# Optimization experiments

Hardware: AMD Instinct MI355X
Metric: run time of the kernel (lower is better)

The kernel has to match this reference:

```python
import jax, jax.numpy as jnp
import numpy as np

LOG2 = float(np.log(2.0))


def setup_inputs() -> dict:
    key = jax.random.key(0)
    ks = jax.random.split(key, 10)
    V, G, F, T = 262144, 4096, 256, 2
    node_feats = jax.random.normal(ks[0], (V, F), dtype=jnp.float32)
    segment_ids = jnp.sort(jax.random.randint(ks[1], (V,), 0, G))
    s = 0.05
    return {
        "node_feats": node_feats,
        "segment_ids": segment_ids,
        "num_graphs": G,
        "logit_w": jax.random.normal(ks[2], (T, 2 * F, 1), dtype=jnp.float32) * s,
        "logit_b": jnp.zeros((T, 1), dtype=jnp.float32),
        "proj_w": jax.random.normal(ks[3], (T, F, F), dtype=jnp.float32) * s,
        "proj_b": jnp.zeros((T, F), dtype=jnp.float32),
        "gru_w_ih": jax.random.normal(ks[4], (T, 3 * F, F), dtype=jnp.float32) * s,
        "gru_w_hh": jax.random.normal(ks[5], (T, 3 * F, F), dtype=jnp.float32) * s,
        "gru_b_ih": jnp.zeros((T, 3 * F), dtype=jnp.float32),
        "gru_b_hh": jnp.zeros((T, 3 * F), dtype=jnp.float32),
    }


def _gru_cell(x, h, w_ih, w_hh, b_ih, b_hh):
    # torch.nn.GRUCell math
    gi = x @ w_ih.T + b_ih  # [G, 3F]
    gh = h @ w_hh.T + b_hh
    i_r, i_z, i_n = jnp.split(gi, 3, axis=-1)
    h_r, h_z, h_n = jnp.split(gh, 3, axis=-1)
    r = jax.nn.sigmoid(i_r + h_r)
    z = jax.nn.sigmoid(i_z + h_z)
    n = jnp.tanh(i_n + r * h_n)
    return (1.0 - z) * n + z * h


def reference(node_feats, segment_ids, num_graphs, logit_w, logit_b,
              proj_w, proj_b, gru_w_ih, gru_w_hh, gru_b_ih, gru_b_hh):
    G = int(num_graphs)
    # initial graph feats: sum of node feats per graph
    g_feats = jax.ops.segment_sum(node_feats, segment_ids, num_segments=G)
    T = logit_w.shape[0]
    for t in range(T):
        # broadcast relu(g_feats) to nodes, concat with node feats, compute logits
        ctx_nodes = jax.nn.relu(g_feats)[segment_ids]              # [V, F]
        z = jnp.concatenate([ctx_nodes, node_feats], axis=-1) @ logit_w[t] + logit_b[t]  # [V,1]
        z = jnp.logaddexp(z, 0.0) - LOG2                           # SoftPlus2
        # segment softmax over nodes within each graph
        zmax = jax.ops.segment_max(z, segment_ids, num_segments=G)
        e = jnp.exp(z - zmax[segment_ids])
        denom = jax.ops.segment_sum(e, segment_ids, num_segments=G)
        a = e / denom[segment_ids]                                 # [V,1]
        # project nodes (dropout=0) and attention-weighted sum per graph
        hv = node_feats @ proj_w[t] + proj_b[t]                    # [V, F]
        g_repr = jax.ops.segment_sum(a * hv, segment_ids, num_segments=G)
        context = jax.nn.elu(g_repr)
        g_feats = _gru_cell(context, g_feats, gru_w_ih[t], gru_w_hh[t], gru_b_ih[t], gru_b_hh[t])
    return g_feats
```

## Files before the change

kernel.cpp:

```cpp
#include <hip/hip_runtime.h>
#include <hip/hip_bf16.h>
#include <math.h>

#define V_NODES 262144
#define NGRAPH  4096
#define FD      256
#define TSTEPS  2

typedef unsigned short u16;
typedef __attribute__((ext_vector_type(8))) short short8;
typedef __attribute__((ext_vector_type(4))) float f32x4;

__device__ __forceinline__ float bf2f(u16 u) {
  union { unsigned int i; float f; } x; x.i = ((unsigned int)u) << 16; return x.f;
}
__device__ __forceinline__ u16 f2bf(float f) {
  union { unsigned int i; float f; } x; x.f = f;
  unsigned int r = x.i + 0x7FFFu + ((x.i >> 16) & 1u);
  return (u16)(r >> 16);
}
__device__ __forceinline__ float softplus2(float x) {
  return fmaxf(x, 0.0f) + log1pf(__expf(-fabsf(x))) - 0.69314718056f;
}

__global__ void k_bounds(const int* __restrict__ seg, int* __restrict__ start) {
  int v = blockIdx.x * blockDim.x + threadIdx.x;
  if (v >= V_NODES) return;
  int s = seg[v];
  if (v == 0) {
    for (int g = 0; g <= s; ++g) start[g] = 0;
  } else {
    int p = seg[v - 1];
    for (int g = p + 1; g <= s; ++g) start[g] = v;
  }
  if (v == V_NODES - 1) {
    for (int g = s + 1; g <= NGRAPH; ++g) start[g] = V_NODES;
  }
}

__global__ __launch_bounds__(256) void k_pass1(
    const float* __restrict__ nf, const int* __restrict__ start,
    const float* __restrict__ logit_w,
    float* __restrict__ gf, u16* __restrict__ nbf,
    u16* __restrict__ hhi, u16* __restrict__ hlo,
    float* __restrict__ d0, float* __restrict__ d1) {
  __shared__ float red[4][FD];
  const int g = blockIdx.x, tid = threadIdx.x;
  const int wv = tid >> 6, l = tid & 63;
  const int s = start[g], e = start[g + 1];
  const float4 wA = ((const float4*)(logit_w + FD))[l];
  const float4 wB = ((const float4*)(logit_w + 512 + FD))[l];
  float a0 = 0.f, a1 = 0.f, a2 = 0.f, a3 = 0.f;
  const float4* nfv = (const float4*)nf;
  ushort4* nbv = (ushort4*)nbf;
  for (int v = s + wv; v < e; v += 4) {
    const float4 x = nfv[(size_t)v * 64 + l];
    a0 += x.x; a1 += x.y; a2 += x.z; a3 += x.w;
    ushort4 ub;
    ub.x = f2bf(x.x); ub.y = f2bf(x.y); ub.z = f2bf(x.z); ub.w = f2bf(x.w);
    nbv[(size_t)v * 64 + l] = ub;
    float dA = fmaf(x.x, wA.x, fmaf(x.y, wA.y, fmaf(x.z, wA.z, x.w * wA.w)));
    float dB = fmaf(x.x, wB.x, fmaf(x.y, wB.y, fmaf(x.z, wB.z, x.w * wB.w)));
#pragma unroll
    for (int off = 1; off < 64; off <<= 1) {
      dA += __shfl_xor(dA, off, 64);
      dB += __shfl_xor(dB, off, 64);
    }
    if (l == 0) { d0[v] = dA; d1[v] = dB; }
  }
  red[wv][l * 4 + 0] = a0; red[wv][l * 4 + 1] = a1;
  red[wv][l * 4 + 2] = a2; red[wv][l * 4 + 3] = a3;
  __syncthreads();
  const float sum = red[0][tid] + red[1][tid] + red[2][tid] + red[3][tid];
  const size_t idx = (size_t)g * FD + tid;
  gf[idx] = sum;
  const u16 hi = f2bf(sum);
  hhi[idx] = hi;
  hlo[idx] = f2bf(sum - bf2f(hi));
}

__global__ __launch_bounds__(256) void k_attnw(
    const int* __restrict__ start, const float* __restrict__ gf,
    const float* __restrict__ lwA, const float* __restrict__ lbp,
    const float* __restrict__ dt, float* __restrict__ abuf,
    float* __restrict__ den) {
  const int tid = threadIdx.x, lane = tid & 63, wv = tid >> 6;
  const int g = blockIdx.x * 4 + wv;
  const int s = start[g], e = start[g + 1];
  const float lb = lbp[0];
  const float4 hv = ((const float4*)(gf + (size_t)g * FD))[lane];
  const float4 wa = ((const float4*)lwA)[lane];
  float c = fmaf(fmaxf(hv.x, 0.f), wa.x, fmaf(fmaxf(hv.y, 0.f), wa.y,
            fmaf(fmaxf(hv.z, 0.f), wa.z, fmaxf(hv.w, 0.f) * wa.w)));
#pragma unroll
  for (int off = 1; off < 64; off <<= 1) c += __shfl_xor(c, off, 64);
  float m = -1e30f;
  for (int v = s + lane; v < e; v += 64) {
    const float z = softplus2(c + dt[v] + lb);
    abuf[v] = z;
    m = fmaxf(m, z);
  }
#pragma unroll
  for (int off = 1; off < 64; off <<= 1) m = fmaxf(m, __shfl_xor(m, off, 64));
  float lsum = 0.f;
  for (int v = s + lane; v < e; v += 64) {
    const float ez = __expf(abuf[v] - m);
    abuf[v] = ez;
    lsum += ez;
  }
#pragma unroll
  for (int off = 1; off < 64; off <<= 1) lsum += __shfl_xor(lsum, off, 64);
  if (lane == 0) den[g] = lsum;
}

__global__ __launch_bounds__(256) void k_wsum(
    const u16* __restrict__ nbf, const int* __restrict__ start,
    const float* __restrict__ abuf, const float* __restrict__ den,
    u16* __restrict__ wnsbf) {
  __shared__ float red[4][FD];
  const int g = blockIdx.x, tid = threadIdx.x;
  const int wv = tid >> 6, lane = tid & 63;
  const int half = lane >> 5, fl = lane & 31;
  const int s = start[g], e = start[g + 1];
  float acc[8];
#pragma unroll
  for (int j = 0; j < 8; ++j) acc[j] = 0.f;
  for (int v0 = s + 2 * wv + half; v0 < e; v0 += 8) {
    const uint4 u = ((const uint4*)(nbf + (size_t)v0 * FD))[fl];
    const float ev = abuf[v0];
    acc[0] = fmaf(ev, bf2f((u16)(u.x & 0xffff)), acc[0]);
    acc[1] = fmaf(ev, bf2f((u16)(u.x >> 16)),    acc[1]);
    acc[2] = fmaf(ev, bf2f((u16)(u.y & 0xffff)), acc[2]);
    acc[3] = fmaf(ev, bf2f((u16)(u.y >> 16)),    acc[3]);
    acc[4] = fmaf(ev, bf2f((u16)(u.z & 0xffff)), acc[4]);
    acc[5] = fmaf(ev, bf2f((u16)(u.z >> 16)),    acc[5]);
    acc[6] = fmaf(ev, bf2f((u16)(u.w & 0xffff)), acc[6]);
    acc[7] = fmaf(ev, bf2f((u16)(u.w >> 16)),    acc[7]);
  }
#pragma unroll
  for (int j = 0; j < 8; ++j) acc[j] += __shfl_xor(acc[j], 32, 64);
  if (half == 0) {
#pragma unroll
    for (int j = 0; j < 8; ++j) red[wv][fl * 8 + j] = acc[j];
  }
  __syncthreads();
  const float num = red[0][tid] + red[1][tid] + red[2][tid] + red[3][tid];
  const float dv = den[g];
  wnsbf[(size_t)g * FD + tid] = f2bf((e > s) ? (num / dv) : 0.0f);
}

__global__ void k_cvt(const float* __restrict__ src, u16* __restrict__ dst, int n4) {
  const int i = blockIdx.x * 256 + threadIdx.x;
  if (i >= n4) return;
  const float4 x = ((const float4*)src)[i];
  ushort4 u;
  u.x = f2bf(x.x); u.y = f2bf(x.y); u.z = f2bf(x.z); u.w = f2bf(x.w);
  ((ushort4*)dst)[i] = u;
}

__global__ void k_cvt_split(const float* __restrict__ src, u16* __restrict__ hi,
                            u16* __restrict__ lo, int n) {
  const int i = blockIdx.x * 256 + threadIdx.x;
  if (i >= n) return;
  const float x = src[i];
  const u16 h = f2bf(x);
  hi[i] = h;
  lo[i] = f2bf(x - bf2f(h));
}

__global__ void k_cvt_t(const float* __restrict__ src, u16* __restrict__ dst) {
  __shared__ float tile[32][33];
  const int t = blockIdx.z;
  const float* S = src + (size_t)t * FD * FD;
  u16* D = dst + (size_t)t * FD * FD;
  const int bx = blockIdx.x, by = blockIdx.y;
  const int tx = threadIdx.x, ty = threadIdx.y;
#pragma unroll
  for (int i = 0; i < 32; i += 8)
    tile[ty + i][tx] = S[(size_t)(by * 32 + ty + i) * FD + bx * 32 + tx];
  __syncthreads();
#pragma unroll
  for (int i = 0; i < 32; i += 8)
    D[(size_t)(bx * 32 + ty + i) * FD + by * 32 + tx] = f2bf(tile[tx][ty + i]);
}

template <int ACT, int OUTBF, int SPLIT>
__global__ __launch_bounds__(256) void k_wgemm(
    const u16* __restrict__ Xhi, const u16* __restrict__ Xlo,
    const u16* __restrict__ Whi, const u16* __restrict__ Wlo,
    const float* __restrict__ bias, float* __restrict__ Yf,
    u16* __restrict__ Ybf, int N) {
  const int tid = threadIdx.x, lane = tid & 63, wave = tid >> 6;
  const int mt = blockIdx.y * 4 + wave;
  const int nt = blockIdx.x;
  const int r = lane & 15, q = lane >> 4;
  const u16* xp = Xhi + (size_t)(mt * 16 + r) * FD + q * 8;
  const u16* wp = Whi + (size_t)(nt * 16 + r) * FD + q * 8;
  f32x4 acc = {0.f, 0.f, 0.f, 0.f};
#pragma unroll
  for (int kt = 0; kt < 8; ++kt) {
    const short8 a = *(const short8*)(xp + kt * 32);
    const short8 b = *(const short8*)(wp + kt * 32);
    acc = __builtin_amdgcn_mfma_f32_16x16x32_bf16(a, b, acc, 0, 0, 0);
  }
  if (SPLIT >= 1) {
    const u16* xp2 = Xlo + (size_t)(mt * 16 + r) * FD + q * 8;
#pragma unroll
    for (int kt = 0; kt < 8; ++kt) {
      const short8 a = *(const short8*)(xp2 + kt * 32);
      const short8 b = *(const short8*)(wp + kt * 32);
      acc = __builtin_amdgcn_mfma_f32_16x16x32_bf16(a, b, acc, 0, 0, 0);
    }
  }
  if (SPLIT >= 2) {
    const u16* wp2 = Wlo + (size_t)(nt * 16 + r) * FD + q * 8;
#pragma unroll
    for (int kt = 0; kt < 8; ++kt) {
      const short8 a = *(const short8*)(xp + kt * 32);
      const short8 b = *(const short8*)(wp2 + kt * 32);
      acc = __builtin_amdgcn_mfma_f32_16x16x32_bf16(a, b, acc, 0, 0, 0);
    }
  }
  const int gcol = nt * 16 + r;
  const float bs = bias[gcol];
  const int row0 = mt * 16 + q * 4;
#pragma unroll
  for (int i = 0; i < 4; ++i) {
    float v = acc[i] + bs;
    if (ACT == 1) v = (v > 0.0f) ? v : expm1f(v);
    if (OUTBF) Ybf[(size_t)(row0 + i) * N + gcol] = f2bf(v);
    else       Yf[(size_t)(row0 + i) * N + gcol] = v;
  }
}

__global__ __launch_bounds__(256) void k_gru(
    const float* __restrict__ gi, const float* __restrict__ gh,
    float* __restrict__ h, u16* __restrict__ hhi, u16* __restrict__ hlo) {
  const int g = blockIdx.x, f = threadIdx.x;
  const float* gir = gi + (size_t)g * 768;
  const float* ghr = gh + (size_t)g * 768;
  const float ir = gir[f], iz = gir[256 + f], in_ = gir[512 + f];
  const float hr = ghr[f], hz = ghr[256 + f], hn = ghr[512 + f];
  const float r = 1.0f / (1.0f + __expf(-(ir + hr)));
  const float z = 1.0f / (1.0f + __expf(-(iz + hz)));
  const float n = tanhf(in_ + r * hn);
  const size_t idx = (size_t)g * FD + f;
  const float hv = h[idx];
  const float hnew = (1.0f - z) * n + z * hv;
  h[idx] = hnew;
  const u16 hb = f2bf(hnew);
  hhi[idx] = hb;
  hlo[idx] = f2bf(hnew - bf2f(hb));
}

extern "C" void kernel_launch(void* const* d_in, const int* in_sizes, int n_in,
                              void* d_out, int out_size, void* d_ws, size_t ws_size,
                              hipStream_t stream) {
  const float* node    = (const float*)d_in[0];
  const int*   seg     = (const int*)d_in[1];
  const float* logit_w = (const float*)d_in[3];
  const float* logit_b = (const float*)d_in[4];
  const float* proj_w  = (const float*)d_in[5];
  const float* proj_b  = (const float*)d_in[6];
  const float* w_ih    = (const float*)d_in[7];
  const float* w_hh    = (const float*)d_in[8];
  const float* b_ih    = (const float*)d_in[9];
  const float* b_hh    = (const float*)d_in[10];
  float* gfeats = (float*)d_out;

  char* p = (char*)d_ws;
  int* start   = (int*)p;  p += (((NGRAPH + 1) * sizeof(int)) + 255) & ~(size_t)255;
  u16* nbf     = (u16*)p;  p += (size_t)V_NODES * FD * 2;
  float* d0    = (float*)p; p += (size_t)V_NODES * 4;
  float* d1    = (float*)p; p += (size_t)V_NODES * 4;
  float* abuf  = (float*)p; p += (size_t)V_NODES * 4;
  float* den   = (float*)p; p += (size_t)NGRAPH * 4;
  u16* hhi     = (u16*)p;  p += (size_t)NGRAPH * FD * 2;
  u16* hlo     = (u16*)p;  p += (size_t)NGRAPH * FD * 2;
  u16* wnsbf   = (u16*)p;  p += (size_t)NGRAPH * FD * 2;
  u16* ctxbf   = (u16*)p;  p += (size_t)NGRAPH * FD * 2;
  float* gi    = (float*)p; p += (size_t)NGRAPH * 768 * 4;
  float* gh    = (float*)p; p += (size_t)NGRAPH * 768 * 4;
  u16* wihbf   = (u16*)p;  p += (size_t)TSTEPS * 768 * FD * 2;
  u16* whhbf   = (u16*)p;  p += (size_t)TSTEPS * 768 * FD * 2;
  u16* whhlo   = (u16*)p;  p += (size_t)TSTEPS * 768 * FD * 2;
  u16* pwtbf   = (u16*)p;  p += (size_t)TSTEPS * FD * FD * 2;
  (void)ws_size; (void)in_sizes; (void)n_in; (void)out_size;

  k_bounds<<<dim3(V_NODES / 256), dim3(256), 0, stream>>>(seg, start);
  k_pass1<<<dim3(NGRAPH), dim3(256), 0, stream>>>(node, start, logit_w,
                                                  gfeats, nbf, hhi, hlo, d0, d1);

  const int nw = TSTEPS * 768 * FD;
  k_cvt<<<dim3(nw / 4 / 256), dim3(256), 0, stream>>>(w_ih, wihbf, nw / 4);
  k_cvt_split<<<dim3(nw / 256), dim3(256), 0, stream>>>(w_hh, whhbf, whhlo, nw);
  k_cvt_t<<<dim3(8, 8, TSTEPS), dim3(32, 8), 0, stream>>>(proj_w, pwtbf);

  for (int t = 0; t < TSTEPS; ++t) {
    k_attnw<<<dim3(NGRAPH / 4), dim3(256), 0, stream>>>(
        start, gfeats, logit_w + (size_t)t * 512, logit_b + t,
        (t == 0) ? d0 : d1, abuf, den);
    k_wsum<<<dim3(NGRAPH), dim3(256), 0, stream>>>(nbf, start, abuf, den, wnsbf);
    k_wgemm<1, 1, 0><<<dim3(FD / 16, NGRAPH / 64), dim3(256), 0, stream>>>(
        wnsbf, nullptr, pwtbf + (size_t)t * FD * FD, nullptr,
        proj_b + (size_t)t * FD, nullptr, ctxbf, FD);
    k_wgemm<0, 0, 0><<<dim3(768 / 16, NGRAPH / 64), dim3(256), 0, stream>>>(
        ctxbf, nullptr, wihbf + (size_t)t * 768 * FD, nullptr,
        b_ih + (size_t)t * 768, gi, nullptr, 768);
    k_wgemm<0, 0, 2><<<dim3(768 / 16, NGRAPH / 64), dim3(256), 0, stream>>>(
        hhi, hlo, whhbf + (size_t)t * 768 * FD, whhlo + (size_t)t * 768 * FD,
        b_hh + (size_t)t * 768, gh, nullptr, 768);
    k_gru<<<dim3(NGRAPH), dim3(256), 0, stream>>>(gi, gh, gfeats, hhi, hlo);
  }
}
```

Before: 643.5 us.

## Fuse all stages into one persistent megakernel with grid-wide barriers

```diff
diff --git a/kernel.cpp b/kernel.cpp
--- a/kernel.cpp
+++ b/kernel.cpp
@@ -6,6 +6,7 @@
 #define NGRAPH  4096
 #define FD      256
 #define TSTEPS  2
+#define NBLK    1024
 
 typedef unsigned short u16;
 typedef __attribute__((ext_vector_type(8))) short short8;
@@ -19,238 +20,288 @@
   unsigned int r = x.i + 0x7FFFu + ((x.i >> 16) & 1u);
   return (u16)(r >> 16);
 }
+__device__ __forceinline__ unsigned int pkbf(float a, float b) {
+  return (unsigned int)f2bf(a) | ((unsigned int)f2bf(b) << 16);
+}
 __device__ __forceinline__ float softplus2(float x) {
   return fmaxf(x, 0.0f) + log1pf(__expf(-fabsf(x))) - 0.69314718056f;
 }
 
-__global__ void k_bounds(const int* __restrict__ seg, int* __restrict__ start) {
-  int v = blockIdx.x * blockDim.x + threadIdx.x;
-  if (v >= V_NODES) return;
-  int s = seg[v];
-  if (v == 0) {
-    for (int g = 0; g <= s; ++g) start[g] = 0;
-  } else {
-    int p = seg[v - 1];
-    for (int g = p + 1; g <= s; ++g) start[g] = v;
-  }
-  if (v == V_NODES - 1) {
-    for (int g = s + 1; g <= NGRAPH; ++g) start[g] = V_NODES;
-  }
-}
-
-__global__ __launch_bounds__(256) void k_pass1(
-    const float* __restrict__ nf, const int* __restrict__ start,
-    const float* __restrict__ logit_w,
-    float* __restrict__ gf, u16* __restrict__ nbf,
-    u16* __restrict__ hhi, u16* __restrict__ hlo,
-    float* __restrict__ d0, float* __restrict__ d1) {
-  __shared__ float red[4][FD];
-  const int g = blockIdx.x, tid = threadIdx.x;
-  const int wv = tid >> 6, l = tid & 63;
-  const int s = start[g], e = start[g + 1];
-  const float4 wA = ((const float4*)(logit_w + FD))[l];
-  const float4 wB = ((const float4*)(logit_w + 512 + FD))[l];
-  float a0 = 0.f, a1 = 0.f, a2 = 0.f, a3 = 0.f;
-  const float4* nfv = (const float4*)nf;
-  ushort4* nbv = (ushort4*)nbf;
-  for (int v = s + wv; v < e; v += 4) {
-    const float4 x = nfv[(size_t)v * 64 + l];
-    a0 += x.x; a1 += x.y; a2 += x.z; a3 += x.w;
-    ushort4 ub;
-    ub.x = f2bf(x.x); ub.y = f2bf(x.y); ub.z = f2bf(x.z); ub.w = f2bf(x.w);
-    nbv[(size_t)v * 64 + l] = ub;
-    float dA = fmaf(x.x, wA.x, fmaf(x.y, wA.y, fmaf(x.z, wA.z, x.w * wA.w)));
-    float dB = fmaf(x.x, wB.x, fmaf(x.y, wB.y, fmaf(x.z, wB.z, x.w * wB.w)));
-#pragma unroll
-    for (int off = 1; off < 64; off <<= 1) {
-      dA += __shfl_xor(dA, off, 64);
-      dB += __shfl_xor(dB, off, 64);
-    }
-    if (l == 0) { d0[v] = dA; d1[v] = dB; }
-  }
-  red[wv][l * 4 + 0] = a0; red[wv][l * 4 + 1] = a1;
-  red[wv][l * 4 + 2] = a2; red[wv][l * 4 + 3] = a3;
+__device__ __forceinline__ void gsync(int* bar, int id) {
   __syncthreads();
-  const float sum = red[0][tid] + red[1][tid] + red[2][tid] + red[3][tid];
-  const size_t idx = (size_t)g * FD + tid;
-  gf[idx] = sum;
-  const u16 hi = f2bf(sum);
-  hhi[idx] = hi;
-  hlo[idx] = f2bf(sum - bf2f(hi));
-}
-
-__global__ __launch_bounds__(256) void k_attnw(
-    const int* __restrict__ start, const float* __restrict__ gf,
-    const float* __restrict__ lwA, const float* __restrict__ lbp,
-    const float* __restrict__ dt, float* __restrict__ abuf,
-    float* __restrict__ den) {
-  const int tid = threadIdx.x, lane = tid & 63, wv = tid >> 6;
-  const int g = blockIdx.x * 4 + wv;
-  const int s = start[g], e = start[g + 1];
-  const float lb = lbp[0];
-  const float4 hv = ((const float4*)(gf + (size_t)g * FD))[lane];
-  const float4 wa = ((const float4*)lwA)[lane];
-  float c = fmaf(fmaxf(hv.x, 0.f), wa.x, fmaf(fmaxf(hv.y, 0.f), wa.y,
-            fmaf(fmaxf(hv.z, 0.f), wa.z, fmaxf(hv.w, 0.f) * wa.w)));
-#pragma unroll
-  for (int off = 1; off < 64; off <<= 1) c += __shfl_xor(c, off, 64);
-  float m = -1e30f;
-  for (int v = s + lane; v < e; v += 64) {
-    const float z = softplus2(c + dt[v] + lb);
-    abuf[v] = z;
-    m = fmaxf(m, z);
-  }
-#pragma unroll
-  for (int off = 1; off < 64; off <<= 1) m = fmaxf(m, __shfl_xor(m, off, 64));
-  float lsum = 0.f;
-  for (int v = s + lane; v < e; v += 64) {
-    const float ez = __expf(abuf[v] - m);
-    abuf[v] = ez;
-    lsum += ez;
-  }
-#pragma unroll
-  for (int off = 1; off < 64; off <<= 1) lsum += __shfl_xor(lsum, off, 64);
-  if (lane == 0) den[g] = lsum;
-}
-
-__global__ __launch_bounds__(256) void k_wsum(
-    const u16* __restrict__ nbf, const int* __restrict__ start,
-    const float* __restrict__ abuf, const float* __restrict__ den,
-    u16* __restrict__ wnsbf) {
-  __shared__ float red[4][FD];
-  const int g = blockIdx.x, tid = threadIdx.x;
-  const int wv = tid >> 6, lane = tid & 63;
-  const int half = lane >> 5, fl = lane & 31;
-  const int s = start[g], e = start[g + 1];
-  float acc[8];
-#pragma unroll
-  for (int j = 0; j < 8; ++j) acc[j] = 0.f;
-  for (int v0 = s + 2 * wv + half; v0 < e; v0 += 8) {
-    const uint4 u = ((const uint4*)(nbf + (size_t)v0 * FD))[fl];
-    const float ev = abuf[v0];
-    acc[0] = fmaf(ev, bf2f((u16)(u.x & 0xffff)), acc[0]);
-    acc[1] = fmaf(ev, bf2f((u16)(u.x >> 16)),    acc[1]);
-    acc[2] = fmaf(ev, bf2f((u16)(u.y & 0xffff)), acc[2]);
-    acc[3] = fmaf(ev, bf2f((u16)(u.y >> 16)),    acc[3]);
-    acc[4] = fmaf(ev, bf2f((u16)(u.z & 0xffff)), acc[4]);
-    acc[5] = fmaf(ev, bf2f((u16)(u.z >> 16)),    acc[5]);
-    acc[6] = fmaf(ev, bf2f((u16)(u.w & 0xffff)), acc[6]);
-    acc[7] = fmaf(ev, bf2f((u16)(u.w >> 16)),    acc[7]);
-  }
-#pragma unroll
-  for (int j = 0; j < 8; ++j) acc[j] += __shfl_xor(acc[j], 32, 64);
-  if (half == 0) {
-#pragma unroll
-    for (int j = 0; j < 8; ++j) red[wv][fl * 8 + j] = acc[j];
+  if (threadIdx.x == 0) {
+    __threadfence();
+    __hip_atomic_fetch_add(&bar[id], 1, __ATOMIC_ACQ_REL, __HIP_MEMORY_SCOPE_AGENT);
+    while (__hip_atomic_load(&bar[id], __ATOMIC_ACQUIRE, __HIP_MEMORY_SCOPE_AGENT) < NBLK)
+      __builtin_amdgcn_s_sleep(2);
+    __threadfence();
   }
   __syncthreads();
-  const float num = red[0][tid] + red[1][tid] + red[2][tid] + red[3][tid];
-  const float dv = den[g];
-  wnsbf[(size_t)g * FD + tid] = f2bf((e > s) ? (num / dv) : 0.0f);
-}
-
-__global__ void k_cvt(const float* __restrict__ src, u16* __restrict__ dst, int n4) {
-  const int i = blockIdx.x * 256 + threadIdx.x;
-  if (i >= n4) return;
-  const float4 x = ((const float4*)src)[i];
-  ushort4 u;
-  u.x = f2bf(x.x); u.y = f2bf(x.y); u.z = f2bf(x.z); u.w = f2bf(x.w);
-  ((ushort4*)dst)[i] = u;
-}
-
-__global__ void k_cvt_split(const float* __restrict__ src, u16* __restrict__ hi,
-                            u16* __restrict__ lo, int n) {
-  const int i = blockIdx.x * 256 + threadIdx.x;
-  if (i >= n) return;
-  const float x = src[i];
-  const u16 h = f2bf(x);
-  hi[i] = h;
-  lo[i] = f2bf(x - bf2f(h));
-}
-
-__global__ void k_cvt_t(const float* __restrict__ src, u16* __restrict__ dst) {
-  __shared__ float tile[32][33];
-  const int t = blockIdx.z;
-  const float* S = src + (size_t)t * FD * FD;
-  u16* D = dst + (size_t)t * FD * FD;
-  const int bx = blockIdx.x, by = blockIdx.y;
-  const int tx = threadIdx.x, ty = threadIdx.y;
-#pragma unroll
-  for (int i = 0; i < 32; i += 8)
-    tile[ty + i][tx] = S[(size_t)(by * 32 + ty + i) * FD + bx * 32 + tx];
-  __syncthreads();
-#pragma unroll
-  for (int i = 0; i < 32; i += 8)
-    D[(size_t)(bx * 32 + ty + i) * FD + by * 32 + tx] = f2bf(tile[tx][ty + i]);
-}
-
-template <int ACT, int OUTBF, int SPLIT>
-__global__ __launch_bounds__(256) void k_wgemm(
-    const u16* __restrict__ Xhi, const u16* __restrict__ Xlo,
-    const u16* __restrict__ Whi, const u16* __restrict__ Wlo,
-    const float* __restrict__ bias, float* __restrict__ Yf,
-    u16* __restrict__ Ybf, int N) {
-  const int tid = threadIdx.x, lane = tid & 63, wave = tid >> 6;
-  const int mt = blockIdx.y * 4 + wave;
-  const int nt = blockIdx.x;
-  const int r = lane & 15, q = lane >> 4;
-  const u16* xp = Xhi + (size_t)(mt * 16 + r) * FD + q * 8;
-  const u16* wp = Whi + (size_t)(nt * 16 + r) * FD + q * 8;
-  f32x4 acc = {0.f, 0.f, 0.f, 0.f};
+}
+
+__device__ __forceinline__ f32x4 mm256(const u16* __restrict__ X,
+                                       const u16* __restrict__ W, f32x4 acc) {
 #pragma unroll
   for (int kt = 0; kt < 8; ++kt) {
-    const short8 a = *(const short8*)(xp + kt * 32);
-    const short8 b = *(const short8*)(wp + kt * 32);
+    const short8 a = *(const short8*)(X + kt * 32);
+    const short8 b = *(const short8*)(W + kt * 32);
     acc = __builtin_amdgcn_mfma_f32_16x16x32_bf16(a, b, acc, 0, 0, 0);
   }
-  if (SPLIT >= 1) {
-    const u16* xp2 = Xlo + (size_t)(mt * 16 + r) * FD + q * 8;
-#pragma unroll
-    for (int kt = 0; kt < 8; ++kt) {
-      const short8 a = *(const short8*)(xp2 + kt * 32);
-      const short8 b = *(const short8*)(wp + kt * 32);
-      acc = __builtin_amdgcn_mfma_f32_16x16x32_bf16(a, b, acc, 0, 0, 0);
-    }
-  }
-  if (SPLIT >= 2) {
-    const u16* wp2 = Wlo + (size_t)(nt * 16 + r) * FD + q * 8;
-#pragma unroll
-    for (int kt = 0; kt < 8; ++kt) {
-      const short8 a = *(const short8*)(xp + kt * 32);
-      const short8 b = *(const short8*)(wp2 + kt * 32);
-      acc = __builtin_amdgcn_mfma_f32_16x16x32_bf16(a, b, acc, 0, 0, 0);
-    }
-  }
-  const int gcol = nt * 16 + r;
-  const float bs = bias[gcol];
-  const int row0 = mt * 16 + q * 4;
-#pragma unroll
-  for (int i = 0; i < 4; ++i) {
-    float v = acc[i] + bs;
-    if (ACT == 1) v = (v > 0.0f) ? v : expm1f(v);
-    if (OUTBF) Ybf[(size_t)(row0 + i) * N + gcol] = f2bf(v);
-    else       Yf[(size_t)(row0 + i) * N + gcol] = v;
-  }
-}
-
-__global__ __launch_bounds__(256) void k_gru(
-    const float* __restrict__ gi, const float* __restrict__ gh,
-    float* __restrict__ h, u16* __restrict__ hhi, u16* __restrict__ hlo) {
-  const int g = blockIdx.x, f = threadIdx.x;
-  const float* gir = gi + (size_t)g * 768;
-  const float* ghr = gh + (size_t)g * 768;
-  const float ir = gir[f], iz = gir[256 + f], in_ = gir[512 + f];
-  const float hr = ghr[f], hz = ghr[256 + f], hn = ghr[512 + f];
-  const float r = 1.0f / (1.0f + __expf(-(ir + hr)));
-  const float z = 1.0f / (1.0f + __expf(-(iz + hz)));
-  const float n = tanhf(in_ + r * hn);
-  const size_t idx = (size_t)g * FD + f;
-  const float hv = h[idx];
-  const float hnew = (1.0f - z) * n + z * hv;
-  h[idx] = hnew;
-  const u16 hb = f2bf(hnew);
-  hhi[idx] = hb;
-  hlo[idx] = f2bf(hnew - bf2f(hb));
+  return acc;
+}
+
+__global__ __launch_bounds__(256, 4) void k_mega(
+    const float* __restrict__ nf, const int* __restrict__ seg,
+    const float* __restrict__ logit_w, const float* __restrict__ logit_b,
+    const float* __restrict__ proj_w, const float* __restrict__ proj_b,
+    const float* __restrict__ w_ih, const float* __restrict__ w_hh,
+    const float* __restrict__ b_ih, const float* __restrict__ b_hh,
+    float* __restrict__ gf, int* __restrict__ bar, int* __restrict__ start,
+    u16* __restrict__ nbf, float* __restrict__ d0, float* __restrict__ d1,
+    float* __restrict__ abuf, u16* __restrict__ hhi, u16* __restrict__ hlo,
+    u16* __restrict__ wnsbf, u16* __restrict__ ctxbf,
+    float* __restrict__ gibuf, float* __restrict__ ghbuf,
+    u16* __restrict__ wihbf, u16* __restrict__ whhbf, u16* __restrict__ whhlo,
+    u16* __restrict__ pwtbf) {
+  __shared__ char smem[8 * FD * 4];
+  __shared__ float sden[4];
+  float* redf = (float*)smem;
+  const int b = blockIdx.x, tid = threadIdx.x;
+  const int gtid = b * 256 + tid;
+  const int lane = tid & 63, wv = tid >> 6;
+
+  {
+    const int v = gtid;
+    const int s = seg[v];
+    if (v == 0) {
+      for (int g = 0; g <= s; ++g) start[g] = 0;
+    } else {
+      const int p = seg[v - 1];
+      for (int g = p + 1; g <= s; ++g) start[g] = v;
+    }
+    if (v == V_NODES - 1)
+      for (int g = s + 1; g <= NGRAPH; ++g) start[g] = V_NODES;
+  }
+  {
+    const int nchunk = TSTEPS * 768 * FD / 4;
+    if (gtid < nchunk) {
+      const float4 x = ((const float4*)w_ih)[gtid];
+      uint2 u; u.x = pkbf(x.x, x.y); u.y = pkbf(x.z, x.w);
+      ((uint2*)wihbf)[gtid] = u;
+      const float4 y = ((const float4*)w_hh)[gtid];
+      uint2 hi_, lo_;
+      const u16 h0 = f2bf(y.x), h1 = f2bf(y.y), h2 = f2bf(y.z), h3 = f2bf(y.w);
+      hi_.x = (unsigned)h0 | ((unsigned)h1 << 16);
+      hi_.y = (unsigned)h2 | ((unsigned)h3 << 16);
+      lo_.x = pkbf(y.x - bf2f(h0), y.y - bf2f(h1));
+      lo_.y = pkbf(y.z - bf2f(h2), y.w - bf2f(h3));
+      ((uint2*)whhbf)[gtid] = hi_;
+      ((uint2*)whhlo)[gtid] = lo_;
+    }
+  }
+  if (b < 2 * 64) {
+    float (*tl)[33] = (float(*)[33])smem;
+    const int t = b >> 6, tile = b & 63, bx = tile & 7, by = tile >> 3;
+    const int tx = tid & 31, ty = tid >> 5;
+    const float* S = proj_w + (size_t)t * FD * FD;
+    u16* D = pwtbf + (size_t)t * FD * FD;
+#pragma unroll
+    for (int i = 0; i < 32; i += 8)
+      tl[ty + i][tx] = S[(size_t)(by * 32 + ty + i) * FD + bx * 32 + tx];
+    __syncthreads();
+#pragma unroll
+    for (int i = 0; i < 32; i += 8)
+      D[(size_t)(bx * 32 + ty + i) * FD + by * 32 + tx] = f2bf(tl[tx][ty + i]);
+  }
+  gsync(bar, 0);
+
+  {
+    const int h = tid >> 5, sl = tid & 31;
+    float wA[8], wB[8];
+    {
+      const float4 a0 = ((const float4*)(logit_w + FD))[2 * sl];
+      const float4 a1 = ((const float4*)(logit_w + FD))[2 * sl + 1];
+      const float4 b0 = ((const float4*)(logit_w + 512 + FD))[2 * sl];
+      const float4 b1 = ((const float4*)(logit_w + 512 + FD))[2 * sl + 1];
+      wA[0]=a0.x; wA[1]=a0.y; wA[2]=a0.z; wA[3]=a0.w;
+      wA[4]=a1.x; wA[5]=a1.y; wA[6]=a1.z; wA[7]=a1.w;
+      wB[0]=b0.x; wB[1]=b0.y; wB[2]=b0.z; wB[3]=b0.w;
+      wB[4]=b1.x; wB[5]=b1.y; wB[6]=b1.z; wB[7]=b1.w;
+    }
+    for (int gl = 0; gl < 4; ++gl) {
+      const int g = b * 4 + gl;
+      const int s = start[g], e = start[g + 1];
+      float ac[8];
+#pragma unroll
+      for (int j = 0; j < 8; ++j) ac[j] = 0.f;
+      const float4* nfv = (const float4*)nf;
+      for (int v = s + h; v < e; v += 8) {
+        const float4 x0 = nfv[(size_t)v * 64 + 2 * sl];
+        const float4 x1 = nfv[(size_t)v * 64 + 2 * sl + 1];
+        ac[0]+=x0.x; ac[1]+=x0.y; ac[2]+=x0.z; ac[3]+=x0.w;
+        ac[4]+=x1.x; ac[5]+=x1.y; ac[6]+=x1.z; ac[7]+=x1.w;
+        uint4 u;
+        u.x = pkbf(x0.x, x0.y); u.y = pkbf(x0.z, x0.w);
+        u.z = pkbf(x1.x, x1.y); u.w = pkbf(x1.z, x1.w);
+        ((uint4*)(nbf + (size_t)v * FD))[sl] = u;
+        float dA = fmaf(x0.x, wA[0], fmaf(x0.y, wA[1], fmaf(x0.z, wA[2], x0.w * wA[3])));
+        dA = fmaf(x1.x, wA[4], fmaf(x1.y, wA[5], fmaf(x1.z, wA[6], fmaf(x1.w, wA[7], dA))));
+        float dB = fmaf(x0.x, wB[0], fmaf(x0.y, wB[1], fmaf(x0.z, wB[2], x0.w * wB[3])));
+        dB = fmaf(x1.x, wB[4], fmaf(x1.y, wB[5], fmaf(x1.z, wB[6], fmaf(x1.w, wB[7], dB))));
+#pragma unroll
+        for (int off = 1; off < 32; off <<= 1) {
+          dA += __shfl_xor(dA, off, 64);
+          dB += __shfl_xor(dB, off, 64);
+        }
+        if (sl == 0) { d0[v] = dA; d1[v] = dB; }
+      }
+      ((float4*)&redf[h * FD + sl * 8])[0] = make_float4(ac[0], ac[1], ac[2], ac[3]);
+      ((float4*)&redf[h * FD + sl * 8])[1] = make_float4(ac[4], ac[5], ac[6], ac[7]);
+      __syncthreads();
+      float sum = 0.f;
+#pragma unroll
+      for (int j = 0; j < 8; ++j) sum += redf[j * FD + tid];
+      const size_t idx = (size_t)g * FD + tid;
+      gf[idx] = sum;
+      const u16 hb = f2bf(sum);
+      hhi[idx] = hb;
+      hlo[idx] = f2bf(sum - bf2f(hb));
+      __syncthreads();
+    }
+  }
+
+  for (int t = 0; t < TSTEPS; ++t) {
+    __syncthreads();
+    {
+      const int g = b * 4 + wv;
+      const int s = start[g], e = start[g + 1];
+      const float lb = logit_b[t];
+      const float* dt = t ? d1 : d0;
+      const float4 hv = ((const float4*)gf)[(size_t)g * 64 + lane];
+      const float4 wa = ((const float4*)(logit_w + (size_t)t * 512))[lane];
+      float c = fmaf(fmaxf(hv.x, 0.f), wa.x, fmaf(fmaxf(hv.y, 0.f), wa.y,
+                fmaf(fmaxf(hv.z, 0.f), wa.z, fmaxf(hv.w, 0.f) * wa.w)));
+#pragma unroll
+      for (int off = 1; off < 64; off <<= 1) c += __shfl_xor(c, off, 64);
+      float m = -1e30f;
+      for (int v = s + lane; v < e; v += 64) {
+        const float z = softplus2(c + dt[v] + lb);
+        abuf[v] = z;
+        m = fmaxf(m, z);
+      }
+#pragma unroll
+      for (int off = 1; off < 64; off <<= 1) m = fmaxf(m, __shfl_xor(m, off, 64));
+      float ls = 0.f;
+      for (int v = s + lane; v < e; v += 64) {
+        const float ez = __expf(abuf[v] - m);
+        abuf[v] = ez;
+        ls += ez;
+      }
+#pragma unroll
+      for (int off = 1; off < 64; off <<= 1) ls += __shfl_xor(ls, off, 64);
+      if (lane == 0) sden[wv] = ls;
+    }
+    __syncthreads();
+    {
+      const int half = lane >> 5, fl = lane & 31;
+      for (int gl = 0; gl < 4; ++gl) {
+        const int g = b * 4 + gl;
+        const int s = start[g], e = start[g + 1];
+        float acc[8];
+#pragma unroll
+        for (int j = 0; j < 8; ++j) acc[j] = 0.f;
+        for (int v0 = s + 2 * wv + half; v0 < e; v0 += 8) {
+          const uint4 u = ((const uint4*)(nbf + (size_t)v0 * FD))[fl];
+          const float ev = abuf[v0];
+          acc[0] = fmaf(ev, bf2f((u16)(u.x & 0xffff)), acc[0]);
+          acc[1] = fmaf(ev, bf2f((u16)(u.x >> 16)),    acc[1]);
+          acc[2] = fmaf(ev, bf2f((u16)(u.y & 0xffff)), acc[2]);
+          acc[3] = fmaf(ev, bf2f((u16)(u.y >> 16)),    acc[3]);
+          acc[4] = fmaf(ev, bf2f((u16)(u.z & 0xffff)), acc[4]);
+          acc[5] = fmaf(ev, bf2f((u16)(u.z >> 16)),    acc[5]);
+          acc[6] = fmaf(ev, bf2f((u16)(u.w & 0xffff)), acc[6]);
+          acc[7] = fmaf(ev, bf2f((u16)(u.w >> 16)),    acc[7]);
+        }
+#pragma unroll
+        for (int j = 0; j < 8; ++j) acc[j] += __shfl_xor(acc[j], 32, 64);
+        if (half == 0) {
+#pragma unroll
+          for (int j = 0; j < 8; ++j) redf[wv * FD + fl * 8 + j] = acc[j];
+        }
+        __syncthreads();
+        const float num = redf[tid] + redf[FD + tid] + redf[2 * FD + tid] + redf[3 * FD + tid];
+        wnsbf[(size_t)g * FD + tid] = f2bf((e > s) ? (num / sden[gl]) : 0.0f);
+        __syncthreads();
+      }
+    }
+    gsync(bar, 1 + t * 3);
+    {
+      const int wid = b * 4 + wv;
+      const int mt = wid >> 4, nt = wid & 15;
+      const int r = lane & 15, q = lane >> 4;
+      f32x4 acc = {0.f, 0.f, 0.f, 0.f};
+      acc = mm256(wnsbf + (size_t)(mt * 16 + r) * FD + q * 8,
+                  pwtbf + (size_t)t * FD * FD + (size_t)(nt * 16 + r) * FD + q * 8, acc);
+      const int gcol = nt * 16 + r;
+      const float bs = proj_b[t * FD + gcol];
+      const int row0 = mt * 16 + q * 4;
+#pragma unroll
+      for (int i = 0; i < 4; ++i) {
+        float v = acc[i] + bs;
+        v = (v > 0.0f) ? v : expm1f(v);
+        ctxbf[(size_t)(row0 + i) * FD + gcol] = f2bf(v);
+      }
+    }
+    gsync(bar, 2 + t * 3);
+    {
+      const int wid = b * 4 + wv;
+      const int r = lane & 15, q = lane >> 4;
+      const u16* wih_t = wihbf + (size_t)t * 768 * FD;
+      const u16* whh_t = whhbf + (size_t)t * 768 * FD;
+      const u16* whl_t = whhlo + (size_t)t * 768 * FD;
+#pragma unroll
+      for (int j = 0; j < 3; ++j) {
+        const int id = wid + j * 4096;
+        const int mt = id & 255, nt = id >> 8;
+        const int gcol = nt * 16 + r;
+        const int row0 = mt * 16 + q * 4;
+        const size_t xoff = (size_t)(mt * 16 + r) * FD + q * 8;
+        const size_t woff = (size_t)gcol * FD + q * 8;
+        f32x4 ai = {0.f, 0.f, 0.f, 0.f};
+        ai = mm256(ctxbf + xoff, wih_t + woff, ai);
+        const float bi = b_ih[t * 768 + gcol];
+#pragma unroll
+        for (int i = 0; i < 4; ++i)
+          gibuf[(size_t)(row0 + i) * 768 + gcol] = ai[i] + bi;
+        f32x4 ah = {0.f, 0.f, 0.f, 0.f};
+        ah = mm256(hhi + xoff, whh_t + woff, ah);
+        ah = mm256(hlo + xoff, whh_t + woff, ah);
+        ah = mm256(hhi + xoff, whl_t + woff, ah);
+        const float bh = b_hh[t * 768 + gcol];
+#pragma unroll
+        for (int i = 0; i < 4; ++i)
+          ghbuf[(size_t)(row0 + i) * 768 + gcol] = ah[i] + bh;
+      }
+    }
+    gsync(bar, 3 + t * 3);
+    for (int gl = 0; gl < 4; ++gl) {
+      const int g = b * 4 + gl;
+      const float* gir = gibuf + (size_t)g * 768;
+      const float* ghr = ghbuf + (size_t)g * 768;
+      const float ir = gir[tid], iz = gir[256 + tid], in_ = gir[512 + tid];
+      const float hr = ghr[tid], hz = ghr[256 + tid], hn = ghr[512 + tid];
+      const float rr = 1.0f / (1.0f + __expf(-(ir + hr)));
+      const float zz = 1.0f / (1.0f + __expf(-(iz + hz)));
+      const float nn = tanhf(in_ + rr * hn);
+      const size_t idx = (size_t)g * FD + tid;
+      const float hv = gf[idx];
+      const float hnew = (1.0f - zz) * nn + zz * hv;
+      gf[idx] = hnew;
+      const u16 hb = f2bf(hnew);
+      hhi[idx] = hb;
+      hlo[idx] = f2bf(hnew - bf2f(hb));
+    }
+  }
 }
 
 extern "C" void kernel_launch(void* const* d_in, const int* in_sizes, int n_in,
@@ -269,47 +320,27 @@
   float* gfeats = (float*)d_out;
 
   char* p = (char*)d_ws;
-  int* start   = (int*)p;  p += (((NGRAPH + 1) * sizeof(int)) + 255) & ~(size_t)255;
-  u16* nbf     = (u16*)p;  p += (size_t)V_NODES * FD * 2;
+  int* bar     = (int*)p;   p += 256;
+  int* start   = (int*)p;   p += (((NGRAPH + 1) * sizeof(int)) + 255) & ~(size_t)255;
+  u16* nbf     = (u16*)p;   p += (size_t)V_NODES * FD * 2;
   float* d0    = (float*)p; p += (size_t)V_NODES * 4;
   float* d1    = (float*)p; p += (size_t)V_NODES * 4;
   float* abuf  = (float*)p; p += (size_t)V_NODES * 4;
-  float* den   = (float*)p; p += (size_t)NGRAPH * 4;
-  u16* hhi     = (u16*)p;  p += (size_t)NGRAPH * FD * 2;
-  u16* hlo     = (u16*)p;  p += (size_t)NGRAPH * FD * 2;
-  u16* wnsbf   = (u16*)p;  p += (size_t)NGRAPH * FD * 2;
-  u16* ctxbf   = (u16*)p;  p += (size_t)NGRAPH * FD * 2;
+  u16* hhi     = (u16*)p;   p += (size_t)NGRAPH * FD * 2;
+  u16* hlo     = (u16*)p;   p += (size_t)NGRAPH * FD * 2;
+  u16* wnsbf   = (u16*)p;   p += (size_t)NGRAPH * FD * 2;
+  u16* ctxbf   = (u16*)p;   p += (size_t)NGRAPH * FD * 2;
   float* gi    = (float*)p; p += (size_t)NGRAPH * 768 * 4;
   float* gh    = (float*)p; p += (size_t)NGRAPH * 768 * 4;
-  u16* wihbf   = (u16*)p;  p += (size_t)TSTEPS * 768 * FD * 2;
-  u16* whhbf   = (u16*)p;  p += (size_t)TSTEPS * 768 * FD * 2;
-  u16* whhlo   = (u16*)p;  p += (size_t)TSTEPS * 768 * FD * 2;
-  u16* pwtbf   = (u16*)p;  p += (size_t)TSTEPS * FD * FD * 2;
+  u16* wihbf   = (u16*)p;   p += (size_t)TSTEPS * 768 * FD * 2;
+  u16* whhbf   = (u16*)p;   p += (size_t)TSTEPS * 768 * FD * 2;
+  u16* whhlo   = (u16*)p;   p += (size_t)TSTEPS * 768 * FD * 2;
+  u16* pwtbf   = (u16*)p;   p += (size_t)TSTEPS * FD * FD * 2;
   (void)ws_size; (void)in_sizes; (void)n_in; (void)out_size;
 
-  k_bounds<<<dim3(V_NODES / 256), dim3(256), 0, stream>>>(seg, start);
-  k_pass1<<<dim3(NGRAPH), dim3(256), 0, stream>>>(node, start, logit_w,
-                                                  gfeats, nbf, hhi, hlo, d0, d1);
-
-  const int nw = TSTEPS * 768 * FD;
-  k_cvt<<<dim3(nw / 4 / 256), dim3(256), 0, stream>>>(w_ih, wihbf, nw / 4);
-  k_cvt_split<<<dim3(nw / 256), dim3(256), 0, stream>>>(w_hh, whhbf, whhlo, nw);
-  k_cvt_t<<<dim3(8, 8, TSTEPS), dim3(32, 8), 0, stream>>>(proj_w, pwtbf);
-
-  for (int t = 0; t < TSTEPS; ++t) {
-    k_attnw<<<dim3(NGRAPH / 4), dim3(256), 0, stream>>>(
-        start, gfeats, logit_w + (size_t)t * 512, logit_b + t,
-        (t == 0) ? d0 : d1, abuf, den);
-    k_wsum<<<dim3(NGRAPH), dim3(256), 0, stream>>>(nbf, start, abuf, den, wnsbf);
-    k_wgemm<1, 1, 0><<<dim3(FD / 16, NGRAPH / 64), dim3(256), 0, stream>>>(
-        wnsbf, nullptr, pwtbf + (size_t)t * FD * FD, nullptr,
-        proj_b + (size_t)t * FD, nullptr, ctxbf, FD);
-    k_wgemm<0, 0, 0><<<dim3(768 / 16, NGRAPH / 64), dim3(256), 0, stream>>>(
-        ctxbf, nullptr, wihbf + (size_t)t * 768 * FD, nullptr,
-        b_ih + (size_t)t * 768, gi, nullptr, 768);
-    k_wgemm<0, 0, 2><<<dim3(768 / 16, NGRAPH / 64), dim3(256), 0, stream>>>(
-        hhi, hlo, whhbf + (size_t)t * 768 * FD, whhlo + (size_t)t * 768 * FD,
-        b_hh + (size_t)t * 768, gh, nullptr, 768);
-    k_gru<<<dim3(NGRAPH), dim3(256), 0, stream>>>(gi, gh, gfeats, hhi, hlo);
-  }
-}
+  hipMemsetAsync(bar, 0, 256, stream);
+  k_mega<<<dim3(NBLK), dim3(256), 0, stream>>>(
+      node, seg, logit_w, logit_b, proj_w, proj_b, w_ih, w_hh, b_ih, b_hh,
+      gfeats, bar, start, nbf, d0, d1, abuf, hhi, hlo, wnsbf, ctxbf,
+      gi, gh, wihbf, whhbf, whhlo, pwtbf);
+}
```

After: 1.860 ms. 189% more time.
